# Optimization experiments

Measured on AMD Instinct MI355X. Metric: run time of the kernel, lower is better.

## Reference

```python
import jax, jax.numpy as jnp
import numpy as np

# ---- static config (mirrors Anchors.__init__ defaults) ----
STRIDES = [8, 16, 32, 64]
SIZES = [32, 64, 128, 256]
RATIOS = np.array([0.5, 1.0, 2.0])
SCALES = np.array([2 ** 0, 2 ** (1.0 / 3.0), 2 ** (2.0 / 3.0)])
FG_IOU, BG_IOU = 0.5, 0.4
VAR_XY, VAR_WH = 0.1, 0.2


def _anchor_wh(box_size, ratios, scales):
    # Faithful to AnchorLayer.generate_anchors
    a = box_size * np.tile(scales, (2, len(ratios))).T  # [K, 2]
    areas = a[:, 0] * a[:, 1]
    rr = np.repeat(ratios, len(scales))
    w = np.sqrt(areas * rr)
    h = w / rr
    return np.stack([w, h], axis=1).astype(np.float32)  # [K, 2]


def _level_anchors(H, W, stride, box_size):
    wh = _anchor_wh(box_size, RATIOS, SCALES)            # [K, 2]
    K = wh.shape[0]
    xs = (np.arange(W, dtype=np.float32) + 0.5) * stride
    ys = (np.arange(H, dtype=np.float32) + 0.5) * stride
    gx, gy = np.meshgrid(xs, ys)                         # [H, W] each
    grid = np.stack([gx, gy], axis=-1)[:, :, None, :]    # [H, W, 1, 2]
    grid = np.broadcast_to(grid, (H, W, K, 2))
    whb = np.broadcast_to(wh[None, None], (H, W, K, 2))
    return np.concatenate([grid, whb], axis=-1).reshape(-1, 4)  # xywh


def make_anchors(feature_shapes):
    levels = [_level_anchors(h, w, s, bs)
              for (h, w), s, bs in zip(feature_shapes, STRIDES, SIZES)]
    anchors = jnp.asarray(np.concatenate(levels, axis=0))  # [A, 4] xywh
    half = anchors[:, 2:] * 0.5
    anchors_xyxy = jnp.concatenate([anchors[:, :2] - half,
                                    anchors[:, :2] + half], axis=-1)
    return anchors, anchors_xyxy


def batch_box_iou(a_xyxy, g_xyxy):
    # a_xyxy: [A, 4], g_xyxy: [B, M, 4] -> [B, A, M]
    lt = jnp.maximum(a_xyxy[None, :, None, :2], g_xyxy[:, None, :, :2])
    rb = jnp.minimum(a_xyxy[None, :, None, 2:], g_xyxy[:, None, :, 2:])
    wh = jnp.clip(rb - lt, 0.0)
    inter = wh[..., 0] * wh[..., 1]
    area_a = (a_xyxy[:, 2] - a_xyxy[:, 0]) * (a_xyxy[:, 3] - a_xyxy[:, 1])
    area_g = (g_xyxy[..., 2] - g_xyxy[..., 0]) * (g_xyxy[..., 3] - g_xyxy[..., 1])
    return inter / (area_a[None, :, None] + area_g[:, None, :] - inter)


def bbox_to_deltas(boxes_xyxy, anchors_xywh):
    # boxes_xyxy: [B, A, 4], anchors_xywh: [A, 4]
    axy, awh = anchors_xywh[:, :2], anchors_xywh[:, 2:]
    cxcy = (boxes_xyxy[..., :2] + boxes_xyxy[..., 2:]) * 0.5
    txy = (cxcy - axy) / (awh * VAR_XY)
    twh = jnp.log((boxes_xyxy[..., 2:] - boxes_xyxy[..., :2]) / awh) / VAR_WH
    return jnp.concatenate([txy, twh], axis=-1)


def setup_inputs() -> dict:
    key = jax.random.key(0)
    ks = jax.random.split(key, 8)
    B, M = 16, 64
    f3 = jax.random.normal(ks[0], (B, 64, 64, 64), dtype=jnp.float32)
    f4 = jax.random.normal(ks[1], (B, 64, 32, 32), dtype=jnp.float32)
    f5 = jax.random.normal(ks[2], (B, 64, 16, 16), dtype=jnp.float32)
    f6 = jax.random.normal(ks[3], (B, 64, 8, 8), dtype=jnp.float32)
    # valid gt boxes in a 512x512 image, xyxy format
    cxy = jax.random.uniform(ks[4], (B, M, 2), minval=60.0, maxval=452.0)
    wh = jax.random.uniform(ks[5], (B, M, 2), minval=10.0, maxval=110.0)
    gt_boxes = jnp.concatenate([cxy - wh * 0.5, cxy + wh * 0.5], axis=-1)
    gt_labels = jax.random.randint(ks[6], (B, M), 1, 21, dtype=jnp.int64)
    return {"f3": f3, "f4": f4, "f5": f5, "f6": f6,
            "gt_boxes": gt_boxes, "gt_labels": gt_labels}


def reference(f3, f4, f5, f6, gt_boxes, gt_labels):
    feats = [f3, f4, f5, f6]
    shapes = [f.shape[-2:] for f in feats]
    anchors, anchors_xyxy = make_anchors(shapes)      # [A,4], [A,4]

    ious = batch_box_iou(anchors_xyxy, gt_boxes)      # [B, A, M]
    best_iou = ious.max(axis=-1)                      # [B, A]
    best_idx = ious.argmax(axis=-1)                   # [B, A]

    mask_bg = best_iou < BG_IOU
    mask_ign = (best_iou > BG_IOU) & (best_iou < FG_IOU)

    labels = jnp.take_along_axis(gt_labels, best_idx, axis=1)     # [B, A]
    labels = jnp.where(mask_ign, -1, labels)
    labels = jnp.where(mask_bg, 0, labels)

    boxes = jnp.take_along_axis(gt_boxes, best_idx[..., None], axis=1)  # [B,A,4]
    loc_targets = bbox_to_deltas(boxes, anchors)      # [B, A, 4]
    cls_targets = labels                              # [B, A]
    return loc_targets, cls_targets
```

## Files before the change

kernel.cpp:

```cpp
#include <hip/hip_runtime.h>
#include <math.h>

#define A_TOTAL 48960
#define M_GT    64
#define B_BATCH 16

__global__ __launch_bounds__(256) void anchors_assign_kernel(
    const float* __restrict__ gt_boxes,
    const int*   __restrict__ gt_labels,
    float* __restrict__ out_loc,
    float* __restrict__ out_cls)
{
    __shared__ float4 sbox[M_GT];
    __shared__ float  sarea[M_GT];
    __shared__ float  slab[M_GT];

    const int b   = blockIdx.y;
    const int tid = threadIdx.x;

    if (tid < M_GT) {
        float4 g = ((const float4*)gt_boxes)[b * M_GT + tid];
        sbox[tid]  = g;
        sarea[tid] = (g.z - g.x) * (g.w - g.y);
        slab[tid]  = (float)gt_labels[b * M_GT + tid];
    }
    __syncthreads();

    const int a = blockIdx.x * 256 + tid;
    if (a >= A_TOTAL) return;

    int local, W, stride, bs;
    if (a < 36864)      { local = a;         W = 64; stride = 8;  bs = 32;  }
    else if (a < 46080) { local = a - 36864; W = 32; stride = 16; bs = 64;  }
    else if (a < 48384) { local = a - 46080; W = 16; stride = 32; bs = 128; }
    else                { local = a - 48384; W = 8;  stride = 64; bs = 256; }

    const int hw = local / 9;
    const int k  = local - hw * 9;
    const int y  = hw / W;
    const int x  = hw - y * W;
    const int r  = k / 3;
    const int s  = k - r * 3;

    const double sc = (s == 0) ? 1.0 : ((s == 1) ? 1.2599210498948732
                                                 : 1.5874010519681994);
    const double rr = (r == 0) ? 0.5 : ((r == 1) ? 1.0 : 2.0);
    const double av   = (double)bs * sc;
    const double area = av * av;
    const double wd   = sqrt(area * rr);
    const double hd   = wd / rr;
    const float aw = (float)wd, ah = (float)hd;

    const float acx = ((float)x + 0.5f) * (float)stride;
    const float acy = ((float)y + 0.5f) * (float)stride;
    const float hx = aw * 0.5f, hy = ah * 0.5f;
    const float ax1 = acx - hx, ay1 = acy - hy;
    const float ax2 = acx + hx, ay2 = acy + hy;
    const float areaA = (ax2 - ax1) * (ay2 - ay1);

    float wx1 = ax1, wy1 = ay1, wx2 = ax2, wy2 = ay2;
    #pragma unroll
    for (int m = 1; m < 64; m <<= 1) {
        wx1 = fminf(wx1, __shfl_xor(wx1, m, 64));
        wy1 = fminf(wy1, __shfl_xor(wy1, m, 64));
        wx2 = fmaxf(wx2, __shfl_xor(wx2, m, 64));
        wy2 = fmaxf(wy2, __shfl_xor(wy2, m, 64));
    }

    const int lane = tid & 63;
    const float4 gb = sbox[lane];
    const bool cand = (fminf(wx2, gb.z) > fmaxf(wx1, gb.x)) &&
                      (fminf(wy2, gb.w) > fmaxf(wy1, gb.y));
    unsigned long long mask = __ballot(cand);

    float b_inter = 0.0f, b_den = 1.0f;
    int   bidx = 0;
    while (mask) {
        const int j = (int)__builtin_ctzll(mask);
        mask &= mask - 1;
        const float4 g = sbox[j];
        const float ltx = fmaxf(ax1, g.x), lty = fmaxf(ay1, g.y);
        const float rbx = fminf(ax2, g.z), rby = fminf(ay2, g.w);
        const float wx = fmaxf(rbx - ltx, 0.0f);
        const float wy = fmaxf(rby - lty, 0.0f);
        const float inter = wx * wy;
        const float den   = (areaA + sarea[j]) - inter;
        if (inter * b_den > b_inter * den) {
            b_inter = inter; b_den = den; bidx = j;
        }
    }
    const float best = b_inter / b_den;

    float lab = slab[bidx];
    if (best > 0.4f && best < 0.5f) lab = -1.0f;
    if (best < 0.4f)                lab = 0.0f;

    const float4 g = sbox[bidx];
    const float gcx = (g.x + g.z) * 0.5f;
    const float gcy = (g.y + g.w) * 0.5f;
    const float tx = (gcx - acx) / (aw * 0.1f);
    const float ty = (gcy - acy) / (ah * 0.1f);
    const float tw = __logf((g.z - g.x) / aw) * 5.0f;
    const float th = __logf((g.w - g.y) / ah) * 5.0f;

    const size_t idx = (size_t)b * A_TOTAL + a;
    ((float4*)out_loc)[idx] = make_float4(tx, ty, tw, th);
    out_cls[idx] = lab;
}

extern "C" void kernel_launch(void* const* d_in, const int* in_sizes, int n_in,
                              void* d_out, int out_size, void* d_ws, size_t ws_size,
                              hipStream_t stream) {
    const float* gt_boxes  = (const float*)d_in[4];
    const int*   gt_labels = (const int*)d_in[5];

    float* out_loc = (float*)d_out;
    float* out_cls = (float*)d_out + (size_t)B_BATCH * A_TOTAL * 4;

    dim3 grid((A_TOTAL + 255) / 256, B_BATCH);
    anchors_assign_kernel<<<grid, 256, 0, stream>>>(gt_boxes, gt_labels, out_loc, out_cls);
}
```

Before: 94.75 us.

## Precompute per-anchor geometry and wave bounds in a prep kernel shared across batch

Adds a prep kernel that computes each anchor's center, size, reciprocals and per-wave bounding window once into workspace. The main kernel then loads these instead of recomputing the double-precision sqrt and shuffle reductions for every batch, and swaps divisions for reciprocal multiplies. This adds a second launch and extra global reads, and the reciprocal multiplies may differ slightly in rounding from true division.

```diff
diff --git a/kernel.cpp b/kernel.cpp
--- a/kernel.cpp
+++ b/kernel.cpp
@@ -2,31 +2,14 @@
 #include <math.h>
 
 #define A_TOTAL 48960
+#define N_WAVES (A_TOTAL / 64)
 #define M_GT    64
 #define B_BATCH 16
 
-__global__ __launch_bounds__(256) void anchors_assign_kernel(
-    const float* __restrict__ gt_boxes,
-    const int*   __restrict__ gt_labels,
-    float* __restrict__ out_loc,
-    float* __restrict__ out_cls)
+__global__ __launch_bounds__(256) void prep_kernel(
+    float4* __restrict__ rec, float4* __restrict__ rin, float4* __restrict__ win)
 {
-    __shared__ float4 sbox[M_GT];
-    __shared__ float  sarea[M_GT];
-    __shared__ float  slab[M_GT];
-
-    const int b   = blockIdx.y;
-    const int tid = threadIdx.x;
-
-    if (tid < M_GT) {
-        float4 g = ((const float4*)gt_boxes)[b * M_GT + tid];
-        sbox[tid]  = g;
-        sarea[tid] = (g.z - g.x) * (g.w - g.y);
-        slab[tid]  = (float)gt_labels[b * M_GT + tid];
-    }
-    __syncthreads();
-
-    const int a = blockIdx.x * 256 + tid;
+    const int a = blockIdx.x * 256 + threadIdx.x;
     if (a >= A_TOTAL) return;
 
     int local, W, stride, bs;
@@ -56,7 +39,10 @@
     const float hx = aw * 0.5f, hy = ah * 0.5f;
     const float ax1 = acx - hx, ay1 = acy - hy;
     const float ax2 = acx + hx, ay2 = acy + hy;
-    const float areaA = (ax2 - ax1) * (ay2 - ay1);
+
+    rec[a] = make_float4(acx, acy, aw, ah);
+    rin[a] = make_float4(1.0f / (aw * 0.1f), 1.0f / (ah * 0.1f),
+                         1.0f / aw,          1.0f / ah);
 
     float wx1 = ax1, wy1 = ay1, wx2 = ax2, wy2 = ay2;
     #pragma unroll
@@ -66,11 +52,50 @@
         wx2 = fmaxf(wx2, __shfl_xor(wx2, m, 64));
         wy2 = fmaxf(wy2, __shfl_xor(wy2, m, 64));
     }
+    if ((threadIdx.x & 63) == 0) win[a >> 6] = make_float4(wx1, wy1, wx2, wy2);
+}
+
+__global__ __launch_bounds__(256) void anchors_assign_kernel(
+    const float*  __restrict__ gt_boxes,
+    const int*    __restrict__ gt_labels,
+    const float4* __restrict__ rec,
+    const float4* __restrict__ rin,
+    const float4* __restrict__ win,
+    float* __restrict__ out_loc,
+    float* __restrict__ out_cls)
+{
+    __shared__ float4 sbox[M_GT];
+    __shared__ float  sarea[M_GT];
+    __shared__ float  slab[M_GT];
+
+    const int b   = blockIdx.y;
+    const int tid = threadIdx.x;
+
+    if (tid < M_GT) {
+        float4 g = ((const float4*)gt_boxes)[b * M_GT + tid];
+        sbox[tid]  = g;
+        sarea[tid] = (g.z - g.x) * (g.w - g.y);
+        slab[tid]  = (float)gt_labels[b * M_GT + tid];
+    }
+    __syncthreads();
+
+    const int a = blockIdx.x * 256 + tid;
+    if (a >= A_TOTAL) return;
+
+    const float4 rc = rec[a];
+    const float4 ri = rin[a];
+    const float4 wv = win[a >> 6];
+
+    const float acx = rc.x, acy = rc.y, aw = rc.z, ah = rc.w;
+    const float hx = aw * 0.5f, hy = ah * 0.5f;
+    const float ax1 = acx - hx, ay1 = acy - hy;
+    const float ax2 = acx + hx, ay2 = acy + hy;
+    const float areaA = (ax2 - ax1) * (ay2 - ay1);
 
     const int lane = tid & 63;
     const float4 gb = sbox[lane];
-    const bool cand = (fminf(wx2, gb.z) > fmaxf(wx1, gb.x)) &&
-                      (fminf(wy2, gb.w) > fmaxf(wy1, gb.y));
+    const bool cand = (fminf(wv.z, gb.z) > fmaxf(wv.x, gb.x)) &&
+                      (fminf(wv.w, gb.w) > fmaxf(wv.y, gb.y));
     unsigned long long mask = __ballot(cand);
 
     float b_inter = 0.0f, b_den = 1.0f;
@@ -98,10 +123,10 @@
     const float4 g = sbox[bidx];
     const float gcx = (g.x + g.z) * 0.5f;
     const float gcy = (g.y + g.w) * 0.5f;
-    const float tx = (gcx - acx) / (aw * 0.1f);
-    const float ty = (gcy - acy) / (ah * 0.1f);
-    const float tw = __logf((g.z - g.x) / aw) * 5.0f;
-    const float th = __logf((g.w - g.y) / ah) * 5.0f;
+    const float tx = (gcx - acx) * ri.x;
+    const float ty = (gcy - acy) * ri.y;
+    const float tw = __logf((g.z - g.x) * ri.z) * 5.0f;
+    const float th = __logf((g.w - g.y) * ri.w) * 5.0f;
 
     const size_t idx = (size_t)b * A_TOTAL + a;
     ((float4*)out_loc)[idx] = make_float4(tx, ty, tw, th);
@@ -114,9 +139,16 @@
     const float* gt_boxes  = (const float*)d_in[4];
     const int*   gt_labels = (const int*)d_in[5];
 
+    float4* rec = (float4*)d_ws;
+    float4* rin = rec + A_TOTAL;
+    float4* win = rin + A_TOTAL;
+
     float* out_loc = (float*)d_out;
     float* out_cls = (float*)d_out + (size_t)B_BATCH * A_TOTAL * 4;
 
+    prep_kernel<<<(A_TOTAL + 255) / 256, 256, 0, stream>>>(rec, rin, win);
+
     dim3 grid((A_TOTAL + 255) / 256, B_BATCH);
-    anchors_assign_kernel<<<grid, 256, 0, stream>>>(gt_boxes, gt_labels, out_loc, out_cls);
+    anchors_assign_kernel<<<grid, 256, 0, stream>>>(gt_boxes, gt_labels,
+                                                    rec, rin, win, out_loc, out_cls);
 }
```

Result: faster. 91.29 us (-3.7%).
